# Kernel tuning notes

Hardware: AMD Instinct MI355X
Metric: run time of the kernel (lower is better)

Reference implementation:

```python
import jax, jax.numpy as jnp
import numpy as np

H = 12  # num_heads


def setup_inputs() -> dict:
    key = jax.random.key(0)
    ks = jax.random.split(key, 5)
    B, N, C = 4, 1025, 768
    x = jax.random.normal(ks[0], (B, N, C), jnp.float32)
    g_info = jax.random.normal(ks[1], (2, 2, C), jnp.float32)
    # parameters (torch Linear equivalents, pre-transposed to x @ W layout)
    w_qkv = jax.random.normal(ks[2], (C, 3 * C), jnp.float32) * (C ** -0.5)
    w_proj = jax.random.normal(ks[3], (C, C), jnp.float32) * (C ** -0.5)
    b_proj = jax.random.normal(ks[4], (C,), jnp.float32) * 0.02
    return {"x": x, "g_info": g_info, "w_qkv": w_qkv, "w_proj": w_proj, "b_proj": b_proj}


def _forward(x, g_info, w_qkv, w_proj, b_proj):
    B, N, C = x.shape
    Dh = C // H
    qkv = (x @ w_qkv).reshape(B, N, 3, H, Dh)
    q, k, v = qkv[:, :, 0], qkv[:, :, 1], qkv[:, :, 2]  # (B,N,H,Dh)

    # grounding query from first g_info layer, row 0
    q_g = g_info[0].reshape(-1, H, Dh)[0]  # (H,Dh)

    # num_reserved = 1 (cls token); "pure" = patch tokens
    q_pure = q[:, 1:]  # (B,M,H,Dh)
    qn = q_pure / jnp.linalg.norm(q_pure, axis=-1, keepdims=True)
    qgn = q_g / jnp.linalg.norm(q_g, axis=-1, keepdims=True)
    q_sim = (qn * qgn).sum(-1).mean(-1)  # (B,M): cosine sim averaged over heads
    q_sim = (q_sim - q_sim.min()) / (q_sim.max() - q_sim.min())  # global min-max norm
    pos = q_sim > 0.9   # (B,M) per-batch routing mask
    neg = ~pos
    # a token index is kept in a group if ANY batch element routes it there
    keep_pos = pos.any(axis=0)  # (M,)
    keep_neg = neg.any(axis=0)

    scale = Dh ** -0.5  # xformers memory_efficient_attention internal scale

    def group_attn(gmask, keep):
        # gmask (B,M) bool; keep (M,) bool. Faithful to the torch gather:
        # kept-but-other-batch tokens participate with ZEROED q/k/v.
        m = gmask[..., None, None].astype(x.dtype)  # (B,M,1,1)
        qg = jnp.concatenate([q[:, :1], q_pure * m], axis=1)      # (B,N,H,Dh)
        kg = jnp.concatenate([k[:, :1], k[:, 1:] * m], axis=1)
        vg = jnp.concatenate([v[:, :1], v[:, 1:] * m], axis=1)
        key_keep = jnp.concatenate([jnp.ones((1,), bool), keep])  # cls always kept
        logits = jnp.einsum('bqhd,bkhd->bhqk', qg, kg) * scale
        logits = jnp.where(key_keep[None, None, None, :], logits, -jnp.inf)
        attn = jax.nn.softmax(logits, axis=-1)
        return jnp.einsum('bhqk,bkhd->bqhd', attn, vg)  # (B,N,H,Dh)

    out_pos = group_attn(pos, keep_pos)
    out_neg = group_attn(neg, keep_neg)

    # indices in neither group stay zero (cannot happen since pos|neg covers all).
    body = jnp.where(keep_neg[None, :, None, None], out_neg[:, 1:],
                     jnp.where(keep_pos[None, :, None, None], out_pos[:, 1:],
                               jnp.zeros_like(out_pos[:, 1:])))
    cls = (out_pos[:, :1] + out_neg[:, :1]) * 0.5
    xo = jnp.concatenate([cls, body], axis=1).reshape(B, N, C)
    return xo @ w_proj + b_proj


def reference(x, g_info, w_qkv, w_proj, b_proj):
    return (_forward(x, g_info, w_qkv, w_proj, b_proj), g_info[1:])
```

## Files before the change

kernel.cpp:

```cpp
#include <hip/hip_runtime.h>
#include <math.h>

typedef unsigned short ushort_t;
typedef short s16x8 __attribute__((ext_vector_type(8)));
typedef float f32x4 __attribute__((ext_vector_type(4)));

#define MFMA16(a, b, c) __builtin_amdgcn_mfma_f32_16x16x32_bf16(a, b, c, 0, 0, 0)

#define BATCH 4
#define SEQ   1025
#define CH    768
#define HEADS 12
#define NBH   48
#define NKPAD 1088
#define NTILE 17
#define NQB   34
#define MROWS 4100
#define SCALE2 0.18033688011112042f

__device__ __forceinline__ ushort_t f2bf(float f) {
    unsigned u = __builtin_bit_cast(unsigned, f);
    u += 0x7FFFu + ((u >> 16) & 1u);
    return (ushort_t)(u >> 16);
}
__device__ __forceinline__ unsigned cvt_pk_bf16(float lo, float hi) {
    unsigned r;
    asm("v_cvt_pk_bf16_f32 %0, %1, %2" : "=v"(r) : "v"(lo), "v"(hi));
    return r;
}
__device__ __forceinline__ float max3f(float a, float b, float c) {
    float r;
    asm("v_max3_f32 %0, %1, %2, %3" : "=v"(r) : "v"(a), "v"(b), "v"(c));
    return r;
}
__device__ __forceinline__ float fast_exp2(float x) {
    float r; asm("v_exp_f32 %0, %1" : "=v"(r) : "v"(x)); return r;
}

__global__ __launch_bounds__(256) void gemm_f32(
    const float* __restrict__ A, const float* __restrict__ Bm,
    float* __restrict__ C0, float* __restrict__ C1,
    int M, int K, int ldb, int Nn)
{
    __shared__ float As[32][68];
    __shared__ float Bs[32][64];
    int t = threadIdx.x;

    int lin = blockIdx.x;
    int xcd = lin & 7, idx = lin >> 3;
    int logical = (xcd < 4 ? xcd * 98 : 392 + (xcd - 4) * 97) + idx;
    int m0 = (logical / 12) * 64, n0 = (logical % 12) * 64;
    int kbase = blockIdx.y * 384;
    float* __restrict__ Cm = blockIdx.y ? C1 : C0;

    int ty = t >> 4, tx = t & 15;
    int laRow = t >> 2, laK = (t & 3) * 4;
    int lbK = t >> 4, lbN = (t & 15) * 4;
    float acc[4][4] = {};
    for (int k0 = kbase; k0 < kbase + 384; k0 += 32) {
        int arow = m0 + laRow;
        #pragma unroll
        for (int half = 0; half < 2; ++half) {
            float4 av = make_float4(0.f, 0.f, 0.f, 0.f);
            if (arow < M) av = *(const float4*)(A + (size_t)arow * K + k0 + laK + 16 * half);
            As[laK + 16 * half + 0][laRow] = av.x;
            As[laK + 16 * half + 1][laRow] = av.y;
            As[laK + 16 * half + 2][laRow] = av.z;
            As[laK + 16 * half + 3][laRow] = av.w;
            *(float4*)&Bs[lbK + 16 * half][lbN] =
                *(const float4*)(Bm + (size_t)(k0 + lbK + 16 * half) * ldb + n0 + lbN);
        }
        __syncthreads();
        #pragma unroll
        for (int kk = 0; kk < 32; ++kk) {
            float4 a4 = *(const float4*)&As[kk][ty * 4];
            float4 b4 = *(const float4*)&Bs[kk][tx * 4];
            float a[4] = {a4.x, a4.y, a4.z, a4.w};
            float b[4] = {b4.x, b4.y, b4.z, b4.w};
            #pragma unroll
            for (int i = 0; i < 4; ++i)
                #pragma unroll
                for (int j = 0; j < 4; ++j) acc[i][j] += a[i] * b[j];
        }
        __syncthreads();
    }
    #pragma unroll
    for (int i = 0; i < 4; ++i) {
        int row = m0 + ty * 4 + i;
        if (row >= M) continue;
        #pragma unroll
        for (int j = 0; j < 4; ++j)
            Cm[(size_t)row * Nn + n0 + tx * 4 + j] = acc[i][j];
    }
}

__global__ __launch_bounds__(256) void convx(const float* __restrict__ x,
                                             ushort_t* __restrict__ xb, int n4)
{
    int i = blockIdx.x * 256 + threadIdx.x;
    if (i >= n4) return;
    float4 v = ((const float4*)x)[i];
    ushort_t o[4] = {f2bf(v.x), f2bf(v.y), f2bf(v.z), f2bf(v.w)};
    *(uint2*)(xb + (size_t)i * 4) = *(const uint2*)o;
}

__global__ __launch_bounds__(256) void convT(const float* __restrict__ src, int ld,
                                             int c0, ushort_t* __restrict__ dst)
{
    __shared__ float tile[32][33];
    int k0 = blockIdx.x * 32, n0 = blockIdx.y * 32;
    int t = threadIdx.x, tx = t & 31, ty = t >> 5;
    #pragma unroll
    for (int i = 0; i < 32; i += 8)
        tile[ty + i][tx] = src[(size_t)(k0 + ty + i) * ld + c0 + n0 + tx];
    __syncthreads();
    #pragma unroll
    for (int i = 0; i < 32; i += 8)
        dst[(size_t)(n0 + ty + i) * CH + k0 + tx] = f2bf(tile[tx][ty + i]);
}

__global__ __launch_bounds__(256) void qconv(const float* __restrict__ q0,
                                             const float* __restrict__ q1,
                                             ushort_t* __restrict__ qtb)
{
    int i = blockIdx.x * 256 + threadIdx.x;
    if (i >= MROWS * CH / 8) return;
    int row = i / (CH / 8);
    int rem = i % (CH / 8);
    int b = row / SEQ, tok = row % SEQ;
    int h = rem >> 3, d8 = (rem & 7) * 8;
    const float* s0 = q0 + (size_t)row * CH + h * 64 + d8;
    const float* s1 = q1 + (size_t)row * CH + h * 64 + d8;
    ushort_t o[8];
    #pragma unroll
    for (int j = 0; j < 8; ++j) o[j] = f2bf(s0[j] + s1[j]);
    *(uint4*)(qtb + ((size_t)(b * HEADS + h) * NKPAD + tok) * 64 + d8) =
        *(const uint4*)o;
}

template<int MODE>
__global__ __launch_bounds__(256) void mfma_gemm(
    const ushort_t* __restrict__ A, const ushort_t* __restrict__ B,
    ushort_t* __restrict__ kbuf, ushort_t* __restrict__ vtbuf,
    const float* __restrict__ bias, float* __restrict__ outp)
{
    __shared__ __align__(16) ushort_t As[128][40];
    __shared__ __align__(16) ushort_t Bs[64][40];
    const int NT = (MODE == 0) ? 24 : 12;
    int t = threadIdx.x, w = t >> 6, l = t & 63;
    int l15 = l & 15, lhi = l >> 4;
    int wr = w >> 1, wc = w & 1;

    int lin = blockIdx.x, logical;
    if (MODE == 0) {
        logical = (lin & 7) * 99 + (lin >> 3);
    } else {
        int xcd = lin & 7, idx = lin >> 3;
        logical = (xcd < 4 ? xcd * 50 : 200 + (xcd - 4) * 49) + idx;
    }
    int m0 = (logical / NT) * 128;
    int n0 = (logical % NT) * 64;

    int trow = t >> 2, tcol = (t & 3) * 8;
    f32x4 acc[4][2] = {};

    for (int k0 = 0; k0 < CH; k0 += 32) {
        uint4 a0v = make_uint4(0, 0, 0, 0), a1v = make_uint4(0, 0, 0, 0);
        int ar0 = m0 + trow, ar1 = m0 + trow + 64;
        if (ar0 < MROWS) a0v = *(const uint4*)(A + (size_t)ar0 * CH + k0 + tcol);
        if (ar1 < MROWS) a1v = *(const uint4*)(A + (size_t)ar1 * CH + k0 + tcol);
        uint4 bv = *(const uint4*)(B + (size_t)(n0 + trow) * CH + k0 + tcol);
        if (k0) __syncthreads();
        *(uint4*)&As[trow][tcol] = a0v;
        *(uint4*)&As[trow + 64][tcol] = a1v;
        *(uint4*)&Bs[trow][tcol] = bv;
        __syncthreads();
        s16x8 af[4], bf[2];
        #pragma unroll
        for (int i = 0; i < 4; ++i)
            af[i] = *(const s16x8*)&As[wr * 64 + 16 * i + l15][lhi * 8];
        #pragma unroll
        for (int j = 0; j < 2; ++j)
            bf[j] = *(const s16x8*)&Bs[wc * 32 + 16 * j + l15][lhi * 8];
        #pragma unroll
        for (int i = 0; i < 4; ++i)
            #pragma unroll
            for (int j = 0; j < 2; ++j)
                acc[i][j] = MFMA16(af[i], bf[j], acc[i][j]);
    }

    #pragma unroll
    for (int i = 0; i < 4; ++i)
        #pragma unroll
        for (int j = 0; j < 2; ++j)
            #pragma unroll
            for (int r = 0; r < 4; ++r) {
                int m = m0 + wr * 64 + 16 * i + lhi * 4 + r;
                if (m >= MROWS) continue;
                int n = n0 + wc * 32 + 16 * j + l15;
                if (MODE == 0) {
                    ushort_t val = f2bf(acc[i][j][r]);
                    int b_ = m / SEQ, tok = m % SEQ;
                    if (n < CH) {
                        int h = n >> 6, d = n & 63;
                        kbuf[((size_t)(b_ * HEADS + h) * NKPAD + tok) * 64 + d] = val;
                    } else {
                        int c = n - CH, h = c >> 6, d = c & 63;
                        vtbuf[((size_t)(b_ * HEADS + h) * 64 + d) * NKPAD + tok] = val;
                    }
                } else {
                    outp[(size_t)m * CH + n] = acc[i][j][r] + bias[n];
                }
            }
}

__global__ __launch_bounds__(256) void zeropad(ushort_t* kbuf, ushort_t* vtbuf, ushort_t* qtb)
{
    int t = blockIdx.x * 256 + threadIdx.x;
    if (t < NBH * 63 * 64) {
        int bh = t / (63 * 64), rem = t % (63 * 64);
        kbuf[((size_t)bh * NKPAD + 1025 + rem / 64) * 64 + (rem & 63)] = 0;
        qtb [((size_t)bh * NKPAD + 1025 + rem / 64) * 64 + (rem & 63)] = 0;
    }
    if (t < NBH * 64 * 63) {
        int bh = t / (64 * 63), rem = t % (64 * 63);
        vtbuf[((size_t)bh * 64 + rem / 63) * NKPAD + 1025 + rem % 63] = 0;
    }
}

__global__ __launch_bounds__(64) void qsim_kernel(
    const float* __restrict__ q0, const float* __restrict__ q1,
    const float* __restrict__ g, float* __restrict__ qsim)
{
    int idx = blockIdx.x;
    int b = idx >> 10, j = idx & 1023, n = j + 1;
    int lane = threadIdx.x;
    const float* r0 = q0 + (size_t)(b * SEQ + n) * CH;
    const float* r1 = q1 + (size_t)(b * SEQ + n) * CH;
    float acc = 0.f;
    for (int h = 0; h < HEADS; ++h) {
        float qv = r0[h * 64 + lane] + r1[h * 64 + lane];
        float gv = g[h * 64 + lane];
        float sqg = qv * gv, sqq = qv * qv, sgg = gv * gv;
        #pragma unroll
        for (int off = 32; off; off >>= 1) {
            sqg += __shfl_xor(sqg, off);
            sqq += __shfl_xor(sqq, off);
            sgg += __shfl_xor(sgg, off);
        }
        acc += sqg / sqrtf(sqq * sgg);
    }
    if (lane == 0) qsim[idx] = acc * (1.0f / HEADS);
}

__global__ __launch_bounds__(1024) void mask_kernel(
    const float* __restrict__ qsim, unsigned char* __restrict__ posm,
    unsigned char* __restrict__ vgrp,
    unsigned long long* __restrict__ actbits, float* __restrict__ n0arr)
{
    __shared__ float wmin[16], wmax[16];
    __shared__ unsigned int sbm[4 * 2 * 34];
    __shared__ int scnt[8];
    int t = threadIdx.x;
    if (t < 4 * 2 * 34) sbm[t] = 0u;
    if (t < 8) scnt[t] = 0;
    float v[4];
    float lmin = 1e30f, lmax = -1e30f;
    #pragma unroll
    for (int b = 0; b < 4; ++b) {
        v[b] = qsim[b * 1024 + t];
        lmin = fminf(lmin, v[b]); lmax = fmaxf(lmax, v[b]);
    }
    #pragma unroll
    for (int off = 32; off; off >>= 1) {
        lmin = fminf(lmin, __shfl_xor(lmin, off));
        lmax = fmaxf(lmax, __shfl_xor(lmax, off));
    }
    if ((t & 63) == 0) { wmin[t >> 6] = lmin; wmax[t >> 6] = lmax; }
    __syncthreads();
    if (t == 0) {
        float gmin = wmin[0], gmax = wmax[0];
        for (int i = 1; i < 16; ++i) { gmin = fminf(gmin, wmin[i]); gmax = fmaxf(gmax, wmax[i]); }
        wmin[0] = gmin; wmax[0] = gmax;
    }
    __syncthreads();
    float gmin = wmin[0], den = wmax[0] - gmin;
    int pb[4], anyp = 0, anyn = 0;
    #pragma unroll
    for (int b = 0; b < 4; ++b) {
        float s = (v[b] - gmin) / den;
        pb[b] = s > 0.9f ? 1 : 0;
        anyp |= pb[b]; anyn |= (1 - pb[b]);
    }
    int k = t + 1;
    int wd = k >> 5;
    unsigned bit = 1u << (k & 31);
    #pragma unroll
    for (int b = 0; b < 4; ++b) {
        if (pb[b]) atomicOr(&sbm[(b * 2 + 0) * 34 + wd], bit);
        else       atomicOr(&sbm[(b * 2 + 1) * 34 + wd], bit);
        unsigned long long bp = __ballot(anyp && !pb[b]);
        unsigned long long bn = __ballot(anyn && pb[b]);
        if ((t & 63) == 0) {
            atomicAdd(&scnt[b * 2 + 0], (int)__popcll(bp));
            atomicAdd(&scnt[b * 2 + 1], (int)__popcll(bn));
        }
        posm[b * 1024 + t] = (unsigned char)pb[b];
    }
    vgrp[2 + t] = (unsigned char)anyn;
    if (t < 2) vgrp[t] = (unsigned char)t;
    if (t < 62) vgrp[1026 + t] = 0;
    __syncthreads();
    if (t < 4 * 2 * 34) {
        unsigned vv = sbm[t];
        if ((t % 34) == 0) vv |= 1u;
        ((unsigned int*)actbits)[t] = vv;
    }
    if (t < 8) n0arr[t] = (float)scnt[t];
}

__global__ __launch_bounds__(256) void attn_mfma(
    const ushort_t* __restrict__ qtb, const ushort_t* __restrict__ kb,
    const ushort_t* __restrict__ vtb,
    const unsigned long long* __restrict__ actbits,
    const float* __restrict__ n0arr,
    const unsigned char* __restrict__ vgrp,
    const unsigned char* __restrict__ posm,
    ushort_t* __restrict__ xob, float* __restrict__ clsf)
{
    __shared__ __align__(16) float comb[4][64][18];

    int t = threadIdx.x, w = t >> 6, l = t & 63;
    int l15 = l & 15, lhi = l >> 4;

    int lin = blockIdx.y * NQB + blockIdx.x;
    int xcd = lin & 7, slot = lin >> 3;
    int bh = xcd * 6 + slot / NQB;
    int qb = slot % NQB;
    int b = bh / HEADS, h = bh % HEADS;

    int qv0 = qb * 32 + l15;
    int qv1 = qv0 + 16;
    int g0 = vgrp[qv0], g1 = vgrp[qv1];
    float n00 = n0arr[b * 2 + g0], n01 = n0arr[b * 2 + g1];
    float mq0 = 1.f, mq1 = 1.f;
    if (qv0 >= 2) {
        int j = qv0 - 2; if (j > 1023) j = 1023;
        int p = posm[b * 1024 + j];
        mq0 = (float)(g0 ? 1 - p : p);
    }
    {
        int j = qv1 - 2; if (j > 1023) j = 1023;
        int p = posm[b * 1024 + j];
        mq1 = (float)(g1 ? 1 - p : p);
    }
    float scl0 = SCALE2 * mq0, scl1 = SCALE2 * mq1;
    const unsigned long long* abp = actbits + (size_t)b * 2 * NTILE;
    const unsigned long long* abn = abp + NTILE;

    int tok0 = (qv0 < 2) ? 0 : qv0 - 1;
    int tok1 = qv1 - 1;
    const ushort_t* qbb = qtb + (size_t)bh * NKPAD * 64 + lhi * 8;
    s16x8 bqA0 = *(const s16x8*)(qbb + (size_t)tok0 * 64);
    s16x8 bqA1 = *(const s16x8*)(qbb + (size_t)tok0 * 64 + 32);
    s16x8 bqB0 = *(const s16x8*)(qbb + (size_t)tok1 * 64);
    s16x8 bqB1 = *(const s16x8*)(qbb + (size_t)tok1 * 64 + 32);

    f32x4 out0[4] = {{0,0,0,0},{0,0,0,0},{0,0,0,0},{0,0,0,0}};
    f32x4 out1[4] = {{0,0,0,0},{0,0,0,0},{0,0,0,0},{0,0,0,0}};
    float mrow0 = -INFINITY, lrow0 = 0.f;
    float mrow1 = -INFINITY, lrow1 = 0.f;

    const ushort_t* kp = kb + (size_t)bh * NKPAD * 64 + (size_t)w * 4096 + l15 * 64 + lhi * 8;
    const ushort_t* vp = vtb + (size_t)bh * 64 * NKPAD + (size_t)l15 * NKPAD + w * 64 + lhi * 8;
    ushort_t* pw = (ushort_t*)&comb[0][0][0] + w * 2048;
    int swz = (l15 & 7) << 3;

    for (int tile = w; tile < NTILE; tile += 4) {
        s16x8 kf[8], vf[8];
        #pragma unroll
        for (int tt = 0; tt < 4; ++tt) {
            kf[2 * tt]     = *(const s16x8*)(kp + 1024 * tt);
            kf[2 * tt + 1] = *(const s16x8*)(kp + 1024 * tt + 32);
        }
        #pragma unroll
        for (int dt = 0; dt < 4; ++dt) {
            const ushort_t* vpd = vp + (size_t)(16 * NKPAD) * dt;
            vf[2 * dt]     = *(const s16x8*)vpd;
            vf[2 * dt + 1] = *(const s16x8*)(vpd + 32);
        }
        f32x4 s0[4], s1[4];
        #pragma unroll
        for (int tt = 0; tt < 4; ++tt) {
            f32x4 a0 = {0, 0, 0, 0}, a1 = {0, 0, 0, 0};
            a0 = MFMA16(kf[2 * tt], bqA0, a0);
            a0 = MFMA16(kf[2 * tt + 1], bqA1, a0);
            a1 = MFMA16(kf[2 * tt], bqB0, a1);
            a1 = MFMA16(kf[2 * tt + 1], bqB1, a1);
            s0[tt] = a0; s1[tt] = a1;
        }
        unsigned long long amp_ = abp[tile], amn_ = abn[tile];
        {
            unsigned long long am = g0 ? amn_ : amp_;
            #pragma unroll
            for (int tt = 0; tt < 4; ++tt) {
                unsigned nib = (unsigned)(am >> (16 * tt + 4 * lhi)) & 0xFu;
                #pragma unroll
                for (int r = 0; r < 4; ++r)
                    s0[tt][r] = ((nib >> r) & 1u) ? s0[tt][r] * scl0 : -INFINITY;
            }
            float ma = max3f(s0[0][0], s0[0][1], s0[0][2]);
            float mb = max3f(s0[0][3], s0[1][0], s0[1][1]);
            float mc = max3f(s0[1][2], s0[1][3], s0[2][0]);
            float md = max3f(s0[2][1], s0[2][2], s0[2][3]);
            float me = max3f(s0[3][0], s0[3][1], s0[3][2]);
            float smax = fmaxf(max3f(ma, mb, mc), max3f(md, me, s0[3][3]));
            smax = fmaxf(smax, __shfl_xor(smax, 16));
            smax = fmaxf(smax, __shfl_xor(smax, 32));
            float mnew = fmaxf(mrow0, smax);
            float msafe = (mnew == -INFINITY) ? 0.f : mnew;
            float alpha = fast_exp2(mrow0 - msafe);
            mrow0 = mnew;
            #pragma unroll
            for (int tt = 0; tt < 4; ++tt)
                #pragma unroll
                for (int r = 0; r < 4; ++r)
                    s0[tt][r] = fast_exp2(s0[tt][r] - msafe);
            float l0 = (s0[0][0] + s0[0][1]) + (s0[0][2] + s0[0][3]);
            float l1 = (s0[1][0] + s0[1][1]) + (s0[1][2] + s0[1][3]);
            float l2 = (s0[2][0] + s0[2][1]) + (s0[2][2] + s0[2][3]);
            float l3 = (s0[3][0] + s0[3][1]) + (s0[3][2] + s0[3][3]);
            float ls = (l0 + l1) + (l2 + l3);
            ls += __shfl_xor(ls, 16);
            ls += __shfl_xor(ls, 32);
            lrow0 = lrow0 * alpha + ls;
            #pragma unroll
            for (int dt = 0; dt < 4; ++dt) out0[dt] *= alpha;
            #pragma unroll
            for (int tt = 0; tt < 4; ++tt) {
                unsigned lo = cvt_pk_bf16(s0[tt][0], s0[tt][1]);
                unsigned hi = cvt_pk_bf16(s0[tt][2], s0[tt][3]);
                int kk = 16 * tt + 4 * lhi;
                *(uint2*)&pw[(l15 * 64 + kk) ^ swz] = make_uint2(lo, hi);
            }
        }
        {
            unsigned long long am = g1 ? amn_ : amp_;
            #pragma unroll
            for (int tt = 0; tt < 4; ++tt) {
                unsigned nib = (unsigned)(am >> (16 * tt + 4 * lhi)) & 0xFu;
                #pragma unroll
                for (int r = 0; r < 4; ++r)
                    s1[tt][r] = ((nib >> r) & 1u) ? s1[tt][r] * scl1 : -INFINITY;
            }
            float ma = max3f(s1[0][0], s1[0][1], s1[0][2]);
            float mb = max3f(s1[0][3], s1[1][0], s1[1][1]);
            float mc = max3f(s1[1][2], s1[1][3], s1[2][0]);
            float md = max3f(s1[2][1], s1[2][2], s1[2][3]);
            float me = max3f(s1[3][0], s1[3][1], s1[3][2]);
            float smax = fmaxf(max3f(ma, mb, mc), max3f(md, me, s1[3][3]));
            smax = fmaxf(smax, __shfl_xor(smax, 16));
            smax = fmaxf(smax, __shfl_xor(smax, 32));
            float mnew = fmaxf(mrow1, smax);
            float msafe = (mnew == -INFINITY) ? 0.f : mnew;
            float alpha = fast_exp2(mrow1 - msafe);
            mrow1 = mnew;
            #pragma unroll
            for (int tt = 0; tt < 4; ++tt)
                #pragma unroll
                for (int r = 0; r < 4; ++r)
                    s1[tt][r] = fast_exp2(s1[tt][r] - msafe);
            float l0 = (s1[0][0] + s1[0][1]) + (s1[0][2] + s1[0][3]);
            float l1 = (s1[1][0] + s1[1][1]) + (s1[1][2] + s1[1][3]);
            float l2 = (s1[2][0] + s1[2][1]) + (s1[2][2] + s1[2][3]);
            float l3 = (s1[3][0] + s1[3][1]) + (s1[3][2] + s1[3][3]);
            float ls = (l0 + l1) + (l2 + l3);
            ls += __shfl_xor(ls, 16);
            ls += __shfl_xor(ls, 32);
            lrow1 = lrow1 * alpha + ls;
            #pragma unroll
            for (int dt = 0; dt < 4; ++dt) out1[dt] *= alpha;
            #pragma unroll
            for (int tt = 0; tt < 4; ++tt) {
                unsigned lo = cvt_pk_bf16(s1[tt][0], s1[tt][1]);
                unsigned hi = cvt_pk_bf16(s1[tt][2], s1[tt][3]);
                int kk = 16 * tt + 4 * lhi;
                *(uint2*)&pw[1024 + ((l15 * 64 + kk) ^ swz)] = make_uint2(lo, hi);
            }
        }
        s16x8 pa0 = *(const s16x8*)&pw[(l15 * 64 + lhi * 8) ^ swz];
        s16x8 pa1 = *(const s16x8*)&pw[(l15 * 64 + 32 + lhi * 8) ^ swz];
        s16x8 pb0 = *(const s16x8*)&pw[1024 + ((l15 * 64 + lhi * 8) ^ swz)];
        s16x8 pb1 = *(const s16x8*)&pw[1024 + ((l15 * 64 + 32 + lhi * 8) ^ swz)];
        #pragma unroll
        for (int dt = 0; dt < 4; ++dt) {
            out0[dt] = MFMA16(vf[2 * dt], pa0, out0[dt]);
            out0[dt] = MFMA16(vf[2 * dt + 1], pa1, out0[dt]);
            out1[dt] = MFMA16(vf[2 * dt], pb0, out1[dt]);
            out1[dt] = MFMA16(vf[2 * dt + 1], pb1, out1[dt]);
        }
        kp += 4 * 4096;
        vp += 4 * 64;
    }

    #pragma unroll
    for (int pass = 0; pass < 2; ++pass) {
        __syncthreads();
        {
            const f32x4* o = pass ? out1 : out0;
            #pragma unroll
            for (int dt = 0; dt < 4; ++dt) *(f32x4*)&comb[w][l][4 * dt] = o[dt];
            comb[w][l][16] = pass ? mrow1 : mrow0;
            comb[w][l][17] = pass ? lrow1 : lrow0;
        }
        __syncthreads();
        if (w == 0) {
            int qv = pass ? qv1 : qv0;
            float n0 = pass ? n01 : n00;
            float M = fmaxf(fmaxf(comb[0][l][16], comb[1][l][16]),
                            fmaxf(comb[2][l][16], comb[3][l][16]));
            if (n0 > 0.f) M = fmaxf(M, 0.f);
            float L = n0 * fast_exp2(0.f - M);
            f32x4 o[4] = {{0,0,0,0},{0,0,0,0},{0,0,0,0},{0,0,0,0}};
            #pragma unroll
            for (int w2 = 0; w2 < 4; ++w2) {
                float a = fast_exp2(comb[w2][l][16] - M);
                L += comb[w2][l][17] * a;
                #pragma unroll
                for (int dt = 0; dt < 4; ++dt)
                    o[dt] += *(const f32x4*)&comb[w2][l][4 * dt] * a;
            }
            float invl = 1.0f / L;
            if (qv <= 1025) {
                if (qv >= 2) {
                    int n = qv - 1;
                    ushort_t* dst = xob + (size_t)(b * SEQ + n) * CH + h * 64 + 4 * lhi;
                    #pragma unroll
                    for (int dt = 0; dt < 4; ++dt) {
                        unsigned lo = cvt_pk_bf16(o[dt][0] * invl, o[dt][1] * invl);
                        unsigned hi = cvt_pk_bf16(o[dt][2] * invl, o[dt][3] * invl);
                        *(uint2*)(dst + 16 * dt) = make_uint2(lo, hi);
                    }
                } else {
                    float* dst = clsf + (size_t)(qv * BATCH + b) * CH + h * 64 + 4 * lhi;
                    #pragma unroll
                    for (int dt = 0; dt < 4; ++dt)
                        #pragma unroll
                        for (int r = 0; r < 4; ++r)
                            dst[16 * dt + r] = o[dt][r] * invl;
                }
            }
        }
    }
}

__global__ __launch_bounds__(768) void cls_combine(
    const float* __restrict__ clsf, ushort_t* __restrict__ xob)
{
    int b = blockIdx.x, c = threadIdx.x;
    float v = 0.5f * (clsf[(size_t)b * CH + c] + clsf[(size_t)(BATCH + b) * CH + c]);
    xob[(size_t)b * SEQ * CH + c] = f2bf(v);
}

extern "C" void kernel_launch(void* const* d_in, const int* in_sizes, int n_in,
                              void* d_out, int out_size, void* d_ws, size_t ws_size,
                              hipStream_t stream) {
    const float* x      = (const float*)d_in[0];
    const float* g_info = (const float*)d_in[1];
    const float* w_qkv  = (const float*)d_in[2];
    const float* w_proj = (const float*)d_in[3];
    const float* b_proj = (const float*)d_in[4];
    float* out = (float*)d_out;
    char* ws = (char*)d_ws;

    size_t off = 0;
    auto alloc = [&](size_t bytes) { size_t o = off; off += (bytes + 255) & ~(size_t)255; return o; };
    float*    qf    = (float*)(ws + alloc((size_t)MROWS * CH * 4));
    ushort_t* xb    = (ushort_t*)(ws + alloc((size_t)MROWS * CH * 2));
    ushort_t* wkvT  = (ushort_t*)(ws + alloc((size_t)2 * CH * CH * 2));
    ushort_t* wpT   = (ushort_t*)(ws + alloc((size_t)CH * CH * 2));
    ushort_t* qtb   = (ushort_t*)(ws + alloc((size_t)NBH * NKPAD * 64 * 2));
    ushort_t* kbuf  = (ushort_t*)(ws + alloc((size_t)NBH * NKPAD * 64 * 2));
    ushort_t* vtbuf = (ushort_t*)(ws + alloc((size_t)NBH * NKPAD * 64 * 2));
    ushort_t* xob   = (ushort_t*)(ws + alloc((size_t)MROWS * CH * 2));
    float*    clsf  = (float*)(ws + alloc((size_t)2 * BATCH * CH * 4));
    float*    qsim  = (float*)(ws + alloc((size_t)BATCH * 1024 * 4));
    unsigned char* posm = (unsigned char*)(ws + alloc((size_t)BATCH * 1024));
    unsigned long long* actbits = (unsigned long long*)(ws + alloc((size_t)BATCH * 2 * NTILE * 8));
    float* n0arr = (float*)(ws + alloc((size_t)8 * 4));
    unsigned char* vgrp = (unsigned char*)(ws + alloc((size_t)NKPAD));

    float* qpart = out;

    convx<<<(MROWS * CH / 4 + 255) / 256, 256, 0, stream>>>(x, xb, MROWS * CH / 4);
    convT<<<dim3(CH / 32, 2 * CH / 32), 256, 0, stream>>>(w_qkv, 3 * CH, CH, wkvT);
    convT<<<dim3(CH / 32, CH / 32), 256, 0, stream>>>(w_proj, CH, 0, wpT);
    zeropad<<<(NBH * 64 * 63 + 255) / 256, 256, 0, stream>>>(kbuf, vtbuf, qtb);

    gemm_f32<<<dim3(780, 2), 256, 0, stream>>>(x, w_qkv, qf, qpart, MROWS, CH, 3 * CH, CH);
    mfma_gemm<0><<<792, 256, 0, stream>>>(xb, wkvT, kbuf, vtbuf, nullptr, nullptr);

    qsim_kernel<<<BATCH * 1024, 64, 0, stream>>>(qf, qpart, g_info, qsim);
    mask_kernel<<<1, 1024, 0, stream>>>(qsim, posm, vgrp, actbits, n0arr);
    qconv<<<(MROWS * CH / 8 + 255) / 256, 256, 0, stream>>>(qf, qpart, qtb);

    attn_mfma<<<dim3(NQB, NBH), 256, 0, stream>>>(
        qtb, kbuf, vtbuf, actbits, n0arr, vgrp, posm, xob, clsf);
    cls_combine<<<BATCH, CH, 0, stream>>>(clsf, xob);

    mfma_gemm<1><<<396, 256, 0, stream>>>(xob, wpT, nullptr, nullptr, b_proj, out);

    hipMemcpyAsync(out + (size_t)MROWS * CH, g_info + 2 * CH, (size_t)2 * CH * sizeof(float),
                   hipMemcpyDeviceToDevice, stream);
}
```

Measured before the change: 232.7 us.

## Merge prep kernels into one launch and co-schedule fp32 Q and bf16 KV GEMMs

```diff
diff --git a/kernel.cpp b/kernel.cpp
--- a/kernel.cpp
+++ b/kernel.cpp
@@ -37,21 +37,67 @@
     float r; asm("v_exp_f32 %0, %1" : "=v"(r) : "v"(x)); return r;
 }
 
-__global__ __launch_bounds__(256) void gemm_f32(
+__global__ __launch_bounds__(256) void prep(
+    const float* __restrict__ x, ushort_t* __restrict__ xb,
+    const float* __restrict__ w_qkv, ushort_t* __restrict__ wkvT,
+    const float* __restrict__ w_proj, ushort_t* __restrict__ wpT,
+    ushort_t* __restrict__ kbuf, ushort_t* __restrict__ vtbuf, ushort_t* __restrict__ qtb)
+{
+    __shared__ float tile[32][33];
+    int b = blockIdx.x, t = threadIdx.x;
+    if (b < 3075) {
+        int i = b * 256 + t;
+        float4 v = ((const float4*)x)[i];
+        ushort_t o[4] = {f2bf(v.x), f2bf(v.y), f2bf(v.z), f2bf(v.w)};
+        *(uint2*)(xb + (size_t)i * 4) = *(const uint2*)o;
+        return;
+    }
+    const float* src; ushort_t* dst; int ld, c0, k0, n0;
+    if (b < 3075 + 1152) {
+        int j = b - 3075;
+        src = w_qkv; dst = wkvT; ld = 3 * CH; c0 = CH;
+        k0 = (j % 24) * 32; n0 = (j / 24) * 32;
+    } else if (b < 3075 + 1152 + 576) {
+        int j = b - 3075 - 1152;
+        src = w_proj; dst = wpT; ld = CH; c0 = 0;
+        k0 = (j % 24) * 32; n0 = (j / 24) * 32;
+    } else {
+        int i = (b - 4803) * 256 + t;
+        {
+            int bh = i / (63 * 64), rem = i % (63 * 64);
+            kbuf[((size_t)bh * NKPAD + 1025 + rem / 64) * 64 + (rem & 63)] = 0;
+            qtb [((size_t)bh * NKPAD + 1025 + rem / 64) * 64 + (rem & 63)] = 0;
+        }
+        {
+            int bh = i / (64 * 63), rem = i % (64 * 63);
+            vtbuf[((size_t)bh * 64 + rem / 63) * NKPAD + 1025 + rem % 63] = 0;
+        }
+        return;
+    }
+    int tx = t & 31, ty = t >> 5;
+    #pragma unroll
+    for (int i = 0; i < 32; i += 8)
+        tile[ty + i][tx] = src[(size_t)(k0 + ty + i) * ld + c0 + n0 + tx];
+    __syncthreads();
+    #pragma unroll
+    for (int i = 0; i < 32; i += 8)
+        dst[(size_t)(n0 + ty + i) * CH + k0 + tx] = f2bf(tile[tx][ty + i]);
+}
+
+
+__device__ __forceinline__ void fp32_body(char* lds, int bx, int slab,
     const float* __restrict__ A, const float* __restrict__ Bm,
-    float* __restrict__ C0, float* __restrict__ C1,
-    int M, int K, int ldb, int Nn)
-{
-    __shared__ float As[32][68];
-    __shared__ float Bs[32][64];
+    float* __restrict__ C0, float* __restrict__ C1)
+{
+    float (*As)[68] = (float(*)[68])lds;
+    float (*Bs)[64] = (float(*)[64])(lds + 32 * 68 * 4);
+    const int M = MROWS, K = CH, ldb = 3 * CH, Nn = CH;
     int t = threadIdx.x;
-
-    int lin = blockIdx.x;
-    int xcd = lin & 7, idx = lin >> 3;
+    int xcd = bx & 7, idx = bx >> 3;
     int logical = (xcd < 4 ? xcd * 98 : 392 + (xcd - 4) * 97) + idx;
     int m0 = (logical / 12) * 64, n0 = (logical % 12) * 64;
-    int kbase = blockIdx.y * 384;
-    float* __restrict__ Cm = blockIdx.y ? C1 : C0;
+    int kbase = slab * 384;
+    float* __restrict__ Cm = slab ? C1 : C0;
 
     int ty = t >> 4, tx = t & 15;
     int laRow = t >> 2, laK = (t & 3) * 4;
@@ -94,70 +140,17 @@
     }
 }
 
-__global__ __launch_bounds__(256) void convx(const float* __restrict__ x,
-                                             ushort_t* __restrict__ xb, int n4)
-{
-    int i = blockIdx.x * 256 + threadIdx.x;
-    if (i >= n4) return;
-    float4 v = ((const float4*)x)[i];
-    ushort_t o[4] = {f2bf(v.x), f2bf(v.y), f2bf(v.z), f2bf(v.w)};
-    *(uint2*)(xb + (size_t)i * 4) = *(const uint2*)o;
-}
-
-__global__ __launch_bounds__(256) void convT(const float* __restrict__ src, int ld,
-                                             int c0, ushort_t* __restrict__ dst)
-{
-    __shared__ float tile[32][33];
-    int k0 = blockIdx.x * 32, n0 = blockIdx.y * 32;
-    int t = threadIdx.x, tx = t & 31, ty = t >> 5;
-    #pragma unroll
-    for (int i = 0; i < 32; i += 8)
-        tile[ty + i][tx] = src[(size_t)(k0 + ty + i) * ld + c0 + n0 + tx];
-    __syncthreads();
-    #pragma unroll
-    for (int i = 0; i < 32; i += 8)
-        dst[(size_t)(n0 + ty + i) * CH + k0 + tx] = f2bf(tile[tx][ty + i]);
-}
-
-__global__ __launch_bounds__(256) void qconv(const float* __restrict__ q0,
-                                             const float* __restrict__ q1,
-                                             ushort_t* __restrict__ qtb)
-{
-    int i = blockIdx.x * 256 + threadIdx.x;
-    if (i >= MROWS * CH / 8) return;
-    int row = i / (CH / 8);
-    int rem = i % (CH / 8);
-    int b = row / SEQ, tok = row % SEQ;
-    int h = rem >> 3, d8 = (rem & 7) * 8;
-    const float* s0 = q0 + (size_t)row * CH + h * 64 + d8;
-    const float* s1 = q1 + (size_t)row * CH + h * 64 + d8;
-    ushort_t o[8];
-    #pragma unroll
-    for (int j = 0; j < 8; ++j) o[j] = f2bf(s0[j] + s1[j]);
-    *(uint4*)(qtb + ((size_t)(b * HEADS + h) * NKPAD + tok) * 64 + d8) =
-        *(const uint4*)o;
-}
-
-template<int MODE>
-__global__ __launch_bounds__(256) void mfma_gemm(
+__device__ __forceinline__ void kv_body(char* lds, int m,
     const ushort_t* __restrict__ A, const ushort_t* __restrict__ B,
-    ushort_t* __restrict__ kbuf, ushort_t* __restrict__ vtbuf,
-    const float* __restrict__ bias, float* __restrict__ outp)
-{
-    __shared__ __align__(16) ushort_t As[128][40];
-    __shared__ __align__(16) ushort_t Bs[64][40];
-    const int NT = (MODE == 0) ? 24 : 12;
+    ushort_t* __restrict__ kbuf, ushort_t* __restrict__ vtbuf)
+{
+    ushort_t (*As)[40] = (ushort_t(*)[40])lds;
+    ushort_t (*Bs)[40] = (ushort_t(*)[40])(lds + 128 * 40 * 2);
+    const int NT = 24;
     int t = threadIdx.x, w = t >> 6, l = t & 63;
     int l15 = l & 15, lhi = l >> 4;
     int wr = w >> 1, wc = w & 1;
-
-    int lin = blockIdx.x, logical;
-    if (MODE == 0) {
-        logical = (lin & 7) * 99 + (lin >> 3);
-    } else {
-        int xcd = lin & 7, idx = lin >> 3;
-        logical = (xcd < 4 ? xcd * 50 : 200 + (xcd - 4) * 49) + idx;
-    }
+    int logical = (m & 7) * 99 + (m >> 3);
     int m0 = (logical / NT) * 128;
     int n0 = (logical % NT) * 64;
 
@@ -195,37 +188,114 @@
         for (int j = 0; j < 2; ++j)
             #pragma unroll
             for (int r = 0; r < 4; ++r) {
+                int mm = m0 + wr * 64 + 16 * i + lhi * 4 + r;
+                if (mm >= MROWS) continue;
+                int n = n0 + wc * 32 + 16 * j + l15;
+                ushort_t val = f2bf(acc[i][j][r]);
+                int b_ = mm / SEQ, tok = mm % SEQ;
+                if (n < CH) {
+                    int h = n >> 6, d = n & 63;
+                    kbuf[((size_t)(b_ * HEADS + h) * NKPAD + tok) * 64 + d] = val;
+                } else {
+                    int c = n - CH, h = c >> 6, d = c & 63;
+                    vtbuf[((size_t)(b_ * HEADS + h) * 64 + d) * NKPAD + tok] = val;
+                }
+            }
+}
+
+__global__ __launch_bounds__(256) void fused_gemms(
+    const float* __restrict__ x, const float* __restrict__ w_qkv,
+    float* __restrict__ q0, float* __restrict__ q1,
+    const ushort_t* __restrict__ xb, const ushort_t* __restrict__ wkvT,
+    ushort_t* __restrict__ kbuf, ushort_t* __restrict__ vtbuf)
+{
+    __shared__ __align__(16) char lds_raw[16896];
+    int lin = blockIdx.x;
+    int q = lin / 3, r3 = lin - 3 * q;
+    if (r3 == 0) {
+        kv_body(lds_raw, q, xb, wkvT, kbuf, vtbuf);
+    } else {
+        int f = q * 2 + (r3 - 1);
+        int bx = f >> 1, slab = f & 1;
+        if (bx >= 780) return;
+        fp32_body(lds_raw, bx, slab, x, w_qkv, q0, q1);
+    }
+}
+
+__global__ __launch_bounds__(256) void qconv(const float* __restrict__ q0,
+                                             const float* __restrict__ q1,
+                                             ushort_t* __restrict__ qtb)
+{
+    int i = blockIdx.x * 256 + threadIdx.x;
+    if (i >= MROWS * CH / 8) return;
+    int row = i / (CH / 8);
+    int rem = i % (CH / 8);
+    int b = row / SEQ, tok = row % SEQ;
+    int h = rem >> 3, d8 = (rem & 7) * 8;
+    const float* s0 = q0 + (size_t)row * CH + h * 64 + d8;
+    const float* s1 = q1 + (size_t)row * CH + h * 64 + d8;
+    ushort_t o[8];
+    #pragma unroll
+    for (int j = 0; j < 8; ++j) o[j] = f2bf(s0[j] + s1[j]);
+    *(uint4*)(qtb + ((size_t)(b * HEADS + h) * NKPAD + tok) * 64 + d8) =
+        *(const uint4*)o;
+}
+
+__global__ __launch_bounds__(256) void projgemm(
+    const ushort_t* __restrict__ A, const ushort_t* __restrict__ B,
+    const float* __restrict__ bias, float* __restrict__ outp)
+{
+    __shared__ __align__(16) ushort_t As[128][40];
+    __shared__ __align__(16) ushort_t Bs[64][40];
+    const int NT = 12;
+    int t = threadIdx.x, w = t >> 6, l = t & 63;
+    int l15 = l & 15, lhi = l >> 4;
+    int wr = w >> 1, wc = w & 1;
+    int lin = blockIdx.x;
+    int xcd = lin & 7, idx = lin >> 3;
+    int logical = (xcd < 4 ? xcd * 50 : 200 + (xcd - 4) * 49) + idx;
+    int m0 = (logical / NT) * 128;
+    int n0 = (logical % NT) * 64;
+
+    int trow = t >> 2, tcol = (t & 3) * 8;
+    f32x4 acc[4][2] = {};
+
+    for (int k0 = 0; k0 < CH; k0 += 32) {
+        uint4 a0v = make_uint4(0, 0, 0, 0), a1v = make_uint4(0, 0, 0, 0);
+        int ar0 = m0 + trow, ar1 = m0 + trow + 64;
+        if (ar0 < MROWS) a0v = *(const uint4*)(A + (size_t)ar0 * CH + k0 + tcol);
+        if (ar1 < MROWS) a1v = *(const uint4*)(A + (size_t)ar1 * CH + k0 + tcol);
+        uint4 bv = *(const uint4*)(B + (size_t)(n0 + trow) * CH + k0 + tcol);
+        if (k0) __syncthreads();
+        *(uint4*)&As[trow][tcol] = a0v;
+        *(uint4*)&As[trow + 64][tcol] = a1v;
+        *(uint4*)&Bs[trow][tcol] = bv;
+        __syncthreads();
+        s16x8 af[4], bf[2];
+        #pragma unroll
+        for (int i = 0; i < 4; ++i)
+            af[i] = *(const s16x8*)&As[wr * 64 + 16 * i + l15][lhi * 8];
+        #pragma unroll
+        for (int j = 0; j < 2; ++j)
+            bf[j] = *(const s16x8*)&Bs[wc * 32 + 16 * j + l15][lhi * 8];
+        #pragma unroll
+        for (int i = 0; i < 4; ++i)
+            #pragma unroll
+            for (int j = 0; j < 2; ++j)
+                acc[i][j] = MFMA16(af[i], bf[j], acc[i][j]);
+    }
+
+    #pragma unroll
+    for (int i = 0; i < 4; ++i)
+        #pragma unroll
+        for (int j = 0; j < 2; ++j)
+            #pragma unroll
+            for (int r = 0; r < 4; ++r) {
                 int m = m0 + wr * 64 + 16 * i + lhi * 4 + r;
                 if (m >= MROWS) continue;
                 int n = n0 + wc * 32 + 16 * j + l15;
-                if (MODE == 0) {
-                    ushort_t val = f2bf(acc[i][j][r]);
-                    int b_ = m / SEQ, tok = m % SEQ;
-                    if (n < CH) {
-                        int h = n >> 6, d = n & 63;
-                        kbuf[((size_t)(b_ * HEADS + h) * NKPAD + tok) * 64 + d] = val;
-                    } else {
-                        int c = n - CH, h = c >> 6, d = c & 63;
-                        vtbuf[((size_t)(b_ * HEADS + h) * 64 + d) * NKPAD + tok] = val;
-                    }
-                } else {
-                    outp[(size_t)m * CH + n] = acc[i][j][r] + bias[n];
-                }
-            }
-}
-
-__global__ __launch_bounds__(256) void zeropad(ushort_t* kbuf, ushort_t* vtbuf, ushort_t* qtb)
-{
-    int t = blockIdx.x * 256 + threadIdx.x;
-    if (t < NBH * 63 * 64) {
-        int bh = t / (63 * 64), rem = t % (63 * 64);
-        kbuf[((size_t)bh * NKPAD + 1025 + rem / 64) * 64 + (rem & 63)] = 0;
-        qtb [((size_t)bh * NKPAD + 1025 + rem / 64) * 64 + (rem & 63)] = 0;
-    }
-    if (t < NBH * 64 * 63) {
-        int bh = t / (64 * 63), rem = t % (64 * 63);
-        vtbuf[((size_t)bh * 64 + rem / 63) * NKPAD + 1025 + rem % 63] = 0;
-    }
+                outp[(size_t)m * CH + n] = acc[i][j][r] + bias[n];
+            }
 }
 
 __global__ __launch_bounds__(64) void qsim_kernel(
@@ -592,13 +662,9 @@
 
     float* qpart = out;
 
-    convx<<<(MROWS * CH / 4 + 255) / 256, 256, 0, stream>>>(x, xb, MROWS * CH / 4);
-    convT<<<dim3(CH / 32, 2 * CH / 32), 256, 0, stream>>>(w_qkv, 3 * CH, CH, wkvT);
-    convT<<<dim3(CH / 32, CH / 32), 256, 0, stream>>>(w_proj, CH, 0, wpT);
-    zeropad<<<(NBH * 64 * 63 + 255) / 256, 256, 0, stream>>>(kbuf, vtbuf, qtb);
-
-    gemm_f32<<<dim3(780, 2), 256, 0, stream>>>(x, w_qkv, qf, qpart, MROWS, CH, 3 * CH, CH);
-    mfma_gemm<0><<<792, 256, 0, stream>>>(xb, wkvT, kbuf, vtbuf, nullptr, nullptr);
+    prep<<<5559, 256, 0, stream>>>(x, xb, w_qkv, wkvT, w_proj, wpT, kbuf, vtbuf, qtb);
+
+    fused_gemms<<<2376, 256, 0, stream>>>(x, w_qkv, qf, qpart, xb, wkvT, kbuf, vtbuf);
 
     qsim_kernel<<<BATCH * 1024, 64, 0, stream>>>(qf, qpart, g_info, qsim);
     mask_kernel<<<1, 1024, 0, stream>>>(qsim, posm, vgrp, actbits, n0arr);
@@ -608,7 +674,7 @@
         qtb, kbuf, vtbuf, actbits, n0arr, vgrp, posm, xob, clsf);
     cls_combine<<<BATCH, CH, 0, stream>>>(clsf, xob);
 
-    mfma_gemm<1><<<396, 256, 0, stream>>>(xob, wpT, nullptr, nullptr, b_proj, out);
+    projgemm<<<396, 256, 0, stream>>>(xob, wpT, b_proj, out);
 
     hipMemcpyAsync(out + (size_t)MROWS * CH, g_info + 2 * CH, (size_t)2 * CH * sizeof(float),
                    hipMemcpyDeviceToDevice, stream);
```

New measurement: 214.6 us. -7.8%, faster.
